# Performance work log

Measured on AMD Instinct MI355X. Metric: run time of the kernel, lower is better.

## Reference

```python
import jax, jax.numpy as jnp
import numpy as np

SIGMA = 0.4            # gaussian geodesic kernel width (class default)
B, N_IN, N_OUT, C, K = 2, 163842, 40962, 128, 7  # icosphere rank 7 -> rank 6, valence-7 candidates


def setup_inputs() -> dict:
    key = jax.random.key(0)
    k_x, k_p, k_o, k_c, k_d = jax.random.split(key, 5)
    x = jax.random.normal(k_x, (B, N_IN, C), dtype=jnp.float32)
    parent_idx = jax.random.randint(k_p, (N_IN,), 0, N_OUT)
    omega = jax.random.uniform(k_o, (N_IN,), dtype=jnp.float32, minval=0.5, maxval=1.5)
    omega = omega / omega.mean()          # matches omega / omega.mean() in __init__
    cand_idx = jax.random.randint(k_c, (N_IN, K), 0, N_OUT)
    cand_mask = jnp.ones((N_IN, K), dtype=jnp.float32)
    delta = jax.random.uniform(k_d, (N_IN, K), dtype=jnp.float32, minval=0.0, maxval=0.5)
    return dict(x=x, omega=omega, delta=delta, cand_mask=cand_mask,
                parent_idx=parent_idx, cand_idx=cand_idx)


def reference(x, omega, delta, cand_mask, parent_idx, cand_idx):
    # --- AreaWeightedDownsample: weight, scatter-add to coarse nodes, normalize ---
    weighted = x * omega[None, :, None]                        # [B, N_in, C]
    down = jnp.zeros((x.shape[0], N_OUT, x.shape[2]), x.dtype)
    down = down.at[:, parent_idx].add(weighted)                # scatter_add over node dim
    denom = jnp.zeros((N_OUT,), x.dtype).at[parent_idx].add(omega)
    down = down / jnp.clip(denom, 1e-8)[None, :, None]         # [B, N_out, C]
    # --- GeodesicKernelUpsample: gather K coarse candidates, gaussian geodesic weights ---
    w = jnp.exp(-(delta * delta) / (2.0 * SIGMA * SIGMA)) * cand_mask   # [N_in, K]
    w = w / jnp.clip(w.sum(axis=-1, keepdims=True), 1e-8)
    gathered = down[:, cand_idx]                               # [B, N_in, K, C]
    return jnp.einsum('nk,bnkc->bnc', w, gathered)             # [B, N_in, C]
```

## Files before the change

kernel.cpp:

```cpp
#include <hip/hip_runtime.h>
#include <hip/hip_bf16.h>

#define B_SZ   2
#define N_IN   163842
#define N_OUT  40962
#define C_DIM  128
#define K_CAND 7
#define INV_2SIG2 3.125f

__global__ __launch_bounds__(256) void count_kernel(
    const int* __restrict__ parent, int* __restrict__ count)
{
    int n = blockIdx.x * 256 + threadIdx.x;
    if (n < N_IN) atomicAdd(&count[parent[n]], 1);
}

__global__ __launch_bounds__(1024) void scan_kernel(
    const int* __restrict__ count, int* __restrict__ offs)
{
    __shared__ int part[1024];
    const int CH = (N_OUT + 1023) / 1024;
    const int t = threadIdx.x;
    const int start = t * CH;

    int s = 0;
    for (int i = 0; i < CH; ++i) {
        int j = start + i;
        if (j < N_OUT) s += count[j];
    }
    part[t] = s;
    __syncthreads();

    for (int off = 1; off < 1024; off <<= 1) {
        int v = (t >= off) ? part[t - off] : 0;
        __syncthreads();
        part[t] += v;
        __syncthreads();
    }

    int run = (t == 0) ? 0 : part[t - 1];
    for (int i = 0; i < CH; ++i) {
        int j = start + i;
        if (j < N_OUT) { offs[j] = run; run += count[j]; }
    }
}

__global__ __launch_bounds__(256) void fill_kernel(
    const int* __restrict__ parent, const int* __restrict__ offs,
    int* __restrict__ cursor, int* __restrict__ perm)
{
    int n = blockIdx.x * 256 + threadIdx.x;
    if (n < N_IN) {
        int p = parent[n];
        int pos = offs[p] + atomicAdd(&cursor[p], 1);
        perm[pos] = n;
    }
}

__global__ __launch_bounds__(C_DIM) void reduce_kernel(
    const float* __restrict__ x,
    const float* __restrict__ omega,
    const int*   __restrict__ offs,
    const int*   __restrict__ perm,
    __hip_bfloat16* __restrict__ down)
{
    const int p = blockIdx.x;
    const int c = threadIdx.x;
    const int beg = offs[p];
    const int end = (p + 1 < N_OUT) ? offs[p + 1] : N_IN;

    float a0 = 0.f, a1 = 0.f, ds = 0.f;
    for (int i = beg; i < end; ++i) {
        const int n = perm[i];
        const float om = omega[n];
        ds += om;
        a0 = fmaf(x[(size_t)n * C_DIM + c], om, a0);
        a1 = fmaf(x[((size_t)N_IN + n) * C_DIM + c], om, a1);
    }
    const float inv = 1.f / fmaxf(ds, 1e-8f);
    down[(size_t)p * C_DIM + c]                 = __float2bfloat16(a0 * inv);
    down[((size_t)N_OUT + p) * C_DIM + c]       = __float2bfloat16(a1 * inv);
}

__global__ __launch_bounds__(256) void gather_kernel(
    const float* __restrict__ delta,
    const float* __restrict__ cand_mask,
    const int*   __restrict__ cand_idx,
    const __hip_bfloat16* __restrict__ down,
    float* __restrict__ out)
{
    const int g    = threadIdx.x >> 6;
    const int lane = threadIdx.x & 63;
    const int n    = blockIdx.x * 4 + g;

    __shared__ float w_sh[4][8];
    __shared__ float coef_sh[4][8];
    __shared__ int   idx_sh[4][8];

    if (n < N_IN && lane < K_CAND) {
        const float d = delta[(size_t)n * K_CAND + lane];
        w_sh[g][lane] = __expf(-d * d * INV_2SIG2) *
                        cand_mask[(size_t)n * K_CAND + lane];
        idx_sh[g][lane] = cand_idx[(size_t)n * K_CAND + lane];
    }
    __syncthreads();
    if (n < N_IN && lane < K_CAND) {
        float s = 0.f;
        #pragma unroll
        for (int k = 0; k < K_CAND; ++k) s += w_sh[g][k];
        coef_sh[g][lane] = w_sh[g][lane] / fmaxf(s, 1e-8f);
    }
    __syncthreads();

    if (n >= N_IN) return;

    const __hip_bfloat162* d2 = (const __hip_bfloat162*)down;
    float2 acc0 = make_float2(0.f, 0.f);
    float2 acc1 = make_float2(0.f, 0.f);
    #pragma unroll
    for (int k = 0; k < K_CAND; ++k) {
        const float cf = coef_sh[g][k];
        const int   p  = idx_sh[g][k];
        const __hip_bfloat162 v0 = d2[(size_t)p * 64 + lane];
        const __hip_bfloat162 v1 = d2[((size_t)N_OUT + p) * 64 + lane];
        acc0.x = fmaf(cf, __bfloat162float(v0.x), acc0.x);
        acc0.y = fmaf(cf, __bfloat162float(v0.y), acc0.y);
        acc1.x = fmaf(cf, __bfloat162float(v1.x), acc1.x);
        acc1.y = fmaf(cf, __bfloat162float(v1.y), acc1.y);
    }
    float2* o2 = (float2*)out;
    o2[(size_t)n * 64 + lane]                 = acc0;
    o2[((size_t)N_IN + n) * 64 + lane]        = acc1;
}

extern "C" void kernel_launch(void* const* d_in, const int* in_sizes, int n_in,
                              void* d_out, int out_size, void* d_ws, size_t ws_size,
                              hipStream_t stream) {
    const float* x         = (const float*)d_in[0];
    const float* omega     = (const float*)d_in[1];
    const float* delta     = (const float*)d_in[2];
    const float* cand_mask = (const float*)d_in[3];
    const int*   parent    = (const int*)d_in[4];
    const int*   cand_idx  = (const int*)d_in[5];
    float* out = (float*)d_out;

    __hip_bfloat16* down = (__hip_bfloat16*)d_ws;
    int* ints   = (int*)(down + (size_t)B_SZ * N_OUT * C_DIM);
    int* count  = ints;
    int* cursor = ints + N_OUT;
    int* offs   = ints + 2 * N_OUT;
    int* perm   = ints + 3 * N_OUT;

    hipMemsetAsync(ints, 0, (size_t)2 * N_OUT * sizeof(int), stream);

    const int nblk = (N_IN + 255) / 256;
    count_kernel<<<nblk, 256, 0, stream>>>(parent, count);
    scan_kernel<<<1, 1024, 0, stream>>>(count, offs);
    fill_kernel<<<nblk, 256, 0, stream>>>(parent, offs, cursor, perm);
    reduce_kernel<<<N_OUT, C_DIM, 0, stream>>>(x, omega, offs, perm, down);
    gather_kernel<<<(N_IN + 3) / 4, 256, 0, stream>>>(
        delta, cand_mask, cand_idx, down, out);
}
```

Measured before the change: 469.8 us.

## Parallelize offset scan across blocks and vectorize reduce with float4 lanes

Replaces the single-block serial-chunk scan with a three-pass multi-block scan (block-local scan, scan of block sums, add-back). The reduce kernel now maps 32 lanes per coarse node with float4 loads and packed bf16x2 stores, so each 256-thread block handles 8 coarse nodes. The aim is to remove the strided serial scan bottleneck and cut per-element load instruction count in the reduce. The cost is two extra kernel launches for the scan.

```diff
diff --git a/kernel.cpp b/kernel.cpp
--- a/kernel.cpp
+++ b/kernel.cpp
@@ -8,6 +8,9 @@
 #define K_CAND 7
 #define INV_2SIG2 3.125f
 
+#define SCAN_B 256
+#define NBLK_SCAN ((N_OUT + SCAN_B - 1) / SCAN_B)
+
 __global__ __launch_bounds__(256) void count_kernel(
     const int* __restrict__ parent, int* __restrict__ count)
 {
@@ -15,34 +18,47 @@
     if (n < N_IN) atomicAdd(&count[parent[n]], 1);
 }
 
-__global__ __launch_bounds__(1024) void scan_kernel(
-    const int* __restrict__ count, int* __restrict__ offs)
-{
-    __shared__ int part[1024];
-    const int CH = (N_OUT + 1023) / 1024;
+__global__ __launch_bounds__(SCAN_B) void scan1_kernel(
+    const int* __restrict__ count, int* __restrict__ offs, int* __restrict__ bsum)
+{
+    __shared__ int sh[SCAN_B];
     const int t = threadIdx.x;
-    const int start = t * CH;
-
-    int s = 0;
-    for (int i = 0; i < CH; ++i) {
-        int j = start + i;
-        if (j < N_OUT) s += count[j];
-    }
-    part[t] = s;
-    __syncthreads();
-
-    for (int off = 1; off < 1024; off <<= 1) {
-        int v = (t >= off) ? part[t - off] : 0;
-        __syncthreads();
-        part[t] += v;
-        __syncthreads();
-    }
-
-    int run = (t == 0) ? 0 : part[t - 1];
-    for (int i = 0; i < CH; ++i) {
-        int j = start + i;
-        if (j < N_OUT) { offs[j] = run; run += count[j]; }
-    }
+    const int j = blockIdx.x * SCAN_B + t;
+    const int c = (j < N_OUT) ? count[j] : 0;
+    sh[t] = c;
+    __syncthreads();
+    for (int off = 1; off < SCAN_B; off <<= 1) {
+        int v = (t >= off) ? sh[t - off] : 0;
+        __syncthreads();
+        sh[t] += v;
+        __syncthreads();
+    }
+    if (j < N_OUT) offs[j] = sh[t] - c;
+    if (t == SCAN_B - 1) bsum[blockIdx.x] = sh[t];
+}
+
+__global__ __launch_bounds__(SCAN_B) void scan2_kernel(
+    const int* __restrict__ bsum, int* __restrict__ bbase)
+{
+    __shared__ int sh[SCAN_B];
+    const int t = threadIdx.x;
+    const int s = (t < NBLK_SCAN) ? bsum[t] : 0;
+    sh[t] = s;
+    __syncthreads();
+    for (int off = 1; off < SCAN_B; off <<= 1) {
+        int v = (t >= off) ? sh[t - off] : 0;
+        __syncthreads();
+        sh[t] += v;
+        __syncthreads();
+    }
+    if (t < NBLK_SCAN) bbase[t] = sh[t] - s;
+}
+
+__global__ __launch_bounds__(SCAN_B) void scan3_kernel(
+    int* __restrict__ offs, const int* __restrict__ bbase)
+{
+    const int j = blockIdx.x * SCAN_B + threadIdx.x;
+    if (j < N_OUT && blockIdx.x > 0) offs[j] += bbase[blockIdx.x];
 }
 
 __global__ __launch_bounds__(256) void fill_kernel(
@@ -57,29 +73,49 @@
     }
 }
 
-__global__ __launch_bounds__(C_DIM) void reduce_kernel(
+__global__ __launch_bounds__(256) void reduce_kernel(
     const float* __restrict__ x,
     const float* __restrict__ omega,
     const int*   __restrict__ offs,
     const int*   __restrict__ perm,
     __hip_bfloat16* __restrict__ down)
 {
-    const int p = blockIdx.x;
-    const int c = threadIdx.x;
+    const int sub = threadIdx.x >> 5;
+    const int l   = threadIdx.x & 31;
+    const int p   = blockIdx.x * 8 + sub;
+    if (p >= N_OUT) return;
+
     const int beg = offs[p];
     const int end = (p + 1 < N_OUT) ? offs[p + 1] : N_IN;
 
-    float a0 = 0.f, a1 = 0.f, ds = 0.f;
+    const float4* x4 = (const float4*)x;
+    float4 a0 = make_float4(0.f, 0.f, 0.f, 0.f);
+    float4 a1 = make_float4(0.f, 0.f, 0.f, 0.f);
+    float ds = 0.f;
+
     for (int i = beg; i < end; ++i) {
         const int n = perm[i];
         const float om = omega[n];
         ds += om;
-        a0 = fmaf(x[(size_t)n * C_DIM + c], om, a0);
-        a1 = fmaf(x[((size_t)N_IN + n) * C_DIM + c], om, a1);
+        const float4 v0 = x4[(size_t)n * 32 + l];
+        const float4 v1 = x4[((size_t)N_IN + n) * 32 + l];
+        a0.x = fmaf(v0.x, om, a0.x); a0.y = fmaf(v0.y, om, a0.y);
+        a0.z = fmaf(v0.z, om, a0.z); a0.w = fmaf(v0.w, om, a0.w);
+        a1.x = fmaf(v1.x, om, a1.x); a1.y = fmaf(v1.y, om, a1.y);
+        a1.z = fmaf(v1.z, om, a1.z); a1.w = fmaf(v1.w, om, a1.w);
     }
     const float inv = 1.f / fmaxf(ds, 1e-8f);
-    down[(size_t)p * C_DIM + c]                 = __float2bfloat16(a0 * inv);
-    down[((size_t)N_OUT + p) * C_DIM + c]       = __float2bfloat16(a1 * inv);
+
+    __hip_bfloat162* d2 = (__hip_bfloat162*)down;
+    __hip_bfloat162 h;
+    h.x = __float2bfloat16(a0.x * inv); h.y = __float2bfloat16(a0.y * inv);
+    d2[(size_t)p * 64 + l * 2] = h;
+    h.x = __float2bfloat16(a0.z * inv); h.y = __float2bfloat16(a0.w * inv);
+    d2[(size_t)p * 64 + l * 2 + 1] = h;
+    h.x = __float2bfloat16(a1.x * inv); h.y = __float2bfloat16(a1.y * inv);
+    d2[((size_t)N_OUT + p) * 64 + l * 2] = h;
+    h.x = __float2bfloat16(a1.z * inv); h.y = __float2bfloat16(a1.w * inv);
+    d2[((size_t)N_OUT + p) * 64 + l * 2 + 1] = h;
 }
 
 __global__ __launch_bounds__(256) void gather_kernel(
@@ -129,8 +165,8 @@
         acc1.y = fmaf(cf, __bfloat162float(v1.y), acc1.y);
     }
     float2* o2 = (float2*)out;
-    o2[(size_t)n * 64 + lane]                 = acc0;
-    o2[((size_t)N_IN + n) * 64 + lane]        = acc1;
+    o2[(size_t)n * 64 + lane]          = acc0;
+    o2[((size_t)N_IN + n) * 64 + lane] = acc1;
 }
 
 extern "C" void kernel_launch(void* const* d_in, const int* in_sizes, int n_in,
@@ -150,14 +186,18 @@
     int* cursor = ints + N_OUT;
     int* offs   = ints + 2 * N_OUT;
     int* perm   = ints + 3 * N_OUT;
+    int* bsum   = perm + N_IN;
+    int* bbase  = bsum + 256;
 
     hipMemsetAsync(ints, 0, (size_t)2 * N_OUT * sizeof(int), stream);
 
     const int nblk = (N_IN + 255) / 256;
     count_kernel<<<nblk, 256, 0, stream>>>(parent, count);
-    scan_kernel<<<1, 1024, 0, stream>>>(count, offs);
+    scan1_kernel<<<NBLK_SCAN, SCAN_B, 0, stream>>>(count, offs, bsum);
+    scan2_kernel<<<1, SCAN_B, 0, stream>>>(bsum, bbase);
+    scan3_kernel<<<NBLK_SCAN, SCAN_B, 0, stream>>>(offs, bbase);
     fill_kernel<<<nblk, 256, 0, stream>>>(parent, offs, cursor, perm);
-    reduce_kernel<<<N_OUT, C_DIM, 0, stream>>>(x, omega, offs, perm, down);
+    reduce_kernel<<<(N_OUT + 7) / 8, 256, 0, stream>>>(x, omega, offs, perm, down);
     gather_kernel<<<(N_IN + 3) / 4, 256, 0, stream>>>(
         delta, cand_mask, cand_idx, down, out);
 }
```

New measurement: 417.2 us. 11.2% less time.
